# Kernel tuning notes

Measured on AMD Instinct MI355X. Metric: run time of the kernel, lower is better.

The kernel has to match this reference:

```python
import jax, jax.numpy as jnp
import numpy as np

L = 6       # n_layers
D = 1024    # d_model
H = 16      # n_heads
HD = D // H
DF = 4096   # d_ff
E = 8       # n_experts
K = 2       # top_k
V = 32000   # vocab
B = 2
S = 1024    # seq_len == max_seq_len


def setup_inputs() -> dict:
    key = jax.random.key(0)
    ks = iter(jax.random.split(key, 40))
    n = lambda shape: jax.random.normal(next(ks), shape, dtype=jnp.float32) * 0.02
    return {
        'input_ids': jax.random.randint(next(ks), (B, S), 0, V),
        'tok_emb': n((V, D)),
        'pos_emb': n((S, D)),
        'attn_in_w': n((L, 3 * D, D)),   # packed q,k,v in_proj (torch MultiheadAttention)
        'attn_in_b': jnp.zeros((L, 3 * D), jnp.float32),
        'attn_out_w': n((L, D, D)),
        'attn_out_b': jnp.zeros((L, D), jnp.float32),
        'ln1_w': jnp.ones((L, D), jnp.float32),
        'ln1_b': jnp.zeros((L, D), jnp.float32),
        'ln2_w': jnp.ones((L, D), jnp.float32),
        'ln2_b': jnp.zeros((L, D), jnp.float32),
        'ffn_w1': n((L, DF, D)),
        'ffn_b1': jnp.zeros((L, DF), jnp.float32),
        'ffn_w2': n((L, D, DF)),
        'ffn_b2': jnp.zeros((L, D), jnp.float32),
        'gate_w': n((L // 2, E, D)),     # router gate for the 3 MoE (odd) layers
        'lnf_w': jnp.ones((D,), jnp.float32),
        'lnf_b': jnp.zeros((D,), jnp.float32),
        'head_w': n((V, D)),
    }


def _ln(x, w, b):
    m = x.mean(-1, keepdims=True)
    v = x.var(-1, keepdims=True)
    return (x - m) / jnp.sqrt(v + 1e-5) * w + b


def _mha(x, in_w, in_b, out_w, out_b):
    b_, s_, _ = x.shape
    qkv = x @ in_w.T + in_b
    q, k, v = jnp.split(qkv, 3, axis=-1)
    rs = lambda t: t.reshape(b_, s_, H, HD)
    q, k, v = rs(q), rs(k), rs(v)
    scores = jnp.einsum('bqhd,bkhd->bhqk', q, k) / np.sqrt(HD).astype(np.float32)
    causal = jnp.tril(jnp.ones((s_, s_), bool))
    scores = jnp.where(causal[None, None], scores, -jnp.inf)
    a = jax.nn.softmax(scores, axis=-1)
    o = jnp.einsum('bhqk,bkhd->bqhd', a, v).reshape(b_, s_, D)
    return o @ out_w.T + out_b


def reference(input_ids, tok_emb, pos_emb, attn_in_w, attn_in_b, attn_out_w,
              attn_out_b, ln1_w, ln1_b, ln2_w, ln2_b, ffn_w1, ffn_b1, ffn_w2,
              ffn_b2, gate_w, lnf_w, lnf_b, head_w):
    s = input_ids.shape[1]
    x = tok_emb[input_ids] + pos_emb[jnp.arange(s)][None]  # [B,S,D]
    aux = jnp.float32(0.0)
    for i in range(L):
        h = _ln(x + _mha(x, attn_in_w[i], attn_in_b[i], attn_out_w[i], attn_out_b[i]),
                ln1_w[i], ln1_b[i])
        ffn = jax.nn.relu(h @ ffn_w1[i].T + ffn_b1[i]) @ ffn_w2[i].T + ffn_b2[i]
        if i % 2 == 1:  # MoE layer; source shares ONE expert module across all experts
            gi = i // 2
            probs = jax.nn.softmax(h @ gate_w[gi].T, axis=-1)     # [B,S,E]
            topv, topi = jax.lax.top_k(probs, K)
            ffn = ffn * topv.sum(-1, keepdims=True)               # combine top-k weights
            me = probs.mean((0, 1))                               # mean gate prob per expert
            ce = jax.nn.one_hot(topi[..., 0], E, dtype=probs.dtype).mean((0, 1))
            aux = aux + E * jnp.sum(me * ce)                      # load-balancing aux loss
        x = _ln(h + ffn, ln2_w[i], ln2_b[i])
    x = _ln(x, lnf_w, lnf_b)
    logits = x @ head_w.T  # [B,S,V]
    return (logits, aux)
```

## Files before the change

### kernel.cpp

```cpp
#include <hip/hip_runtime.h>
#include <hip/hip_bf16.h>

typedef __hip_bfloat16 bf16;
typedef __bf16 bf16x8 __attribute__((ext_vector_type(8)));
typedef float f32x4 __attribute__((ext_vector_type(4)));
typedef short s16x8 __attribute__((ext_vector_type(8)));
typedef unsigned short u16;

#define NL 6
#define DM 1024
#define NH 16
#define HD 64
#define DF 4096
#define NE 8
#define NV 32000
#define NB 2
#define NS 1024
#define NT (NB*NS)

__device__ __forceinline__ float ldin(const void* p, long i, int isf32) {
    return isf32 ? ((const float*)p)[i]
                 : __bfloat162float(((const bf16*)p)[i]);
}

__global__ __launch_bounds__(256)
void cvt_k(const void* __restrict__ src, bf16* __restrict__ dst, long n,
           const u16* __restrict__ probe)
{
    int isf32 = (probe[0] != (u16)0x3F80);
    long stride = (long)gridDim.x * 256 * 8;
    for (long i = ((long)blockIdx.x * 256 + threadIdx.x) * 8; i < n; i += stride) {
        if (isf32) {
            const float* s = (const float*)src + i;
            f32x4 f0 = *(const f32x4*)s;
            f32x4 f1 = *(const f32x4*)(s + 4);
            s16x8 o;
            #pragma unroll
            for (int jj = 0; jj < 4; ++jj) {
                bf16 v0 = __float2bfloat16(f0[jj]);
                bf16 v1 = __float2bfloat16(f1[jj]);
                o[jj]   = *(short*)&v0;
                o[4+jj] = *(short*)&v1;
            }
            *(s16x8*)&dst[i] = o;
        } else {
            *(s16x8*)&dst[i] = *(const s16x8*)((const u16*)src + i);
        }
    }
}

template<int TMI, int WF32, int WB16, int RELU>
__global__ __launch_bounds__(256)
void gemm128(const u16* __restrict__ A, const u16* __restrict__ B,
             const void* __restrict__ bias, long biasoff,
             const u16* __restrict__ probe,
             float* __restrict__ Cf, bf16* __restrict__ Cb,
             int M, int N, int K, int lda, int ldb, int ldc, float alpha)
{
    int isf32 = (probe[0] != (u16)0x3F80);
    int bm = blockIdx.x, bn = blockIdx.y;

    __shared__ __align__(16) u16 As[TMI*32*64];
    __shared__ __align__(16) u16 Bs[128*64];

    int t = threadIdx.x;
    int lane = t & 63, wv = t >> 6;
    int wr = wv >> 1, wc = wv & 1;
    int rsel = lane & 15, grp = lane >> 4;

    f32x4 acc[TMI][4] = {};

    const u16* Ag = A + (long)(bm * (TMI*32)) * lda;
    const u16* Bg = B + (long)(bn * 128) * ldb;
    int sub = lane >> 3;
    int csw = ((lane & 7) ^ sub) * 8;

    for (int kt = 0; kt < K; kt += 64) {
        __syncthreads();
        #pragma unroll
        for (int i = 0; i < TMI; ++i) {
            int row = wv*(TMI*8) + i*8;
            __builtin_amdgcn_global_load_lds(
                (const __attribute__((address_space(1))) void*)(Ag + (long)(row + sub)*lda + kt + csw),
                (__attribute__((address_space(3))) void*)(As + row*64),
                16, 0, 0);
        }
        #pragma unroll
        for (int i = 0; i < 4; ++i) {
            int row = wv*32 + i*8;
            __builtin_amdgcn_global_load_lds(
                (const __attribute__((address_space(1))) void*)(Bg + (long)(row + sub)*ldb + kt + csw),
                (__attribute__((address_space(3))) void*)(Bs + row*64),
                16, 0, 0);
        }
        __syncthreads();
        #pragma unroll
        for (int kk = 0; kk < 2; ++kk) {
            int js = ((kk*4 + grp) ^ (rsel & 7)) * 8;
            bf16x8 af[TMI], bf[4];
            #pragma unroll
            for (int mi = 0; mi < TMI; ++mi)
                af[mi] = *(const bf16x8*)&As[(wr*(TMI*16) + mi*16 + rsel)*64 + js];
            #pragma unroll
            for (int ni = 0; ni < 4; ++ni)
                bf[ni] = *(const bf16x8*)&Bs[(wc*64 + ni*16 + rsel)*64 + js];
            #pragma unroll
            for (int mi = 0; mi < TMI; ++mi)
                #pragma unroll
                for (int ni = 0; ni < 4; ++ni)
                    acc[mi][ni] = __builtin_amdgcn_mfma_f32_16x16x32_bf16(
                        af[mi], bf[ni], acc[mi][ni], 0, 0, 0);
        }
    }

    #pragma unroll
    for (int mi = 0; mi < TMI; ++mi)
    #pragma unroll
    for (int ni = 0; ni < 4; ++ni)
    #pragma unroll
    for (int j = 0; j < 4; ++j) {
        int row = bm*(TMI*32) + wr*(TMI*16) + mi*16 + grp*4 + j;
        int col = bn*128 + wc*64 + ni*16 + rsel;
        float v = acc[mi][ni][j] * alpha;
        if (bias) v += ldin(bias, biasoff + col, isf32);
        if (RELU) v = fmaxf(v, 0.f);
        long ci = (long)row * ldc + col;
        if (WF32) Cf[ci] = v;
        if (WB16) Cb[ci] = __float2bfloat16(v);
    }
}

__global__ __launch_bounds__(256)
void gemm64f(const u16* __restrict__ A, const void* __restrict__ B,
             const u16* __restrict__ probe, float* __restrict__ Cf,
             int M, int N, int K, int lda, int ldb, int ldc)
{
    int isf32 = (probe[0] != (u16)0x3F80);
    int bn = blockIdx.x, bm = blockIdx.y;
    __shared__ __align__(16) u16 As[64*72];
    __shared__ __align__(16) u16 Bs[64*72];
    int t = threadIdx.x;
    int lane = t & 63, wv = t >> 6;
    int wm = (wv >> 1) * 32, wn = (wv & 1) * 32;
    int rsel = lane & 15, grp = lane >> 4;
    f32x4 acc[2][2] = {};
    const u16* Ag = A + (long)(bm * 64) * lda;
    int r0 = t >> 3, c8 = (t & 7) * 8;
    for (int kt = 0; kt < K; kt += 64) {
        __syncthreads();
        #pragma unroll
        for (int p = 0; p < 2; ++p) {
            int r = r0 + 32 * p;
            *(s16x8*)&As[r*72 + c8] = *(const s16x8*)(Ag + (long)r * lda + kt + c8);
        }
        if (isf32) {
            const float* Bg = (const float*)B + (long)(bn * 64) * ldb;
            #pragma unroll
            for (int p = 0; p < 2; ++p) {
                int r = r0 + 32 * p;
                const float* src = Bg + (long)r * ldb + kt + c8;
                f32x4 f0 = *(const f32x4*)src;
                f32x4 f1 = *(const f32x4*)(src + 4);
                s16x8 o8;
                #pragma unroll
                for (int jj = 0; jj < 4; ++jj) {
                    bf16 v0 = __float2bfloat16(f0[jj]);
                    bf16 v1 = __float2bfloat16(f1[jj]);
                    o8[jj]   = *(short*)&v0;
                    o8[4+jj] = *(short*)&v1;
                }
                *(s16x8*)&Bs[r*72 + c8] = o8;
            }
        } else {
            const u16* Bg = (const u16*)B + (long)(bn * 64) * ldb;
            #pragma unroll
            for (int p = 0; p < 2; ++p) {
                int r = r0 + 32 * p;
                *(s16x8*)&Bs[r*72 + c8] = *(const s16x8*)(Bg + (long)r * ldb + kt + c8);
            }
        }
        __syncthreads();
        #pragma unroll
        for (int kk = 0; kk < 64; kk += 32) {
            bf16x8 a0 = *(const bf16x8*)&As[(wm +      rsel)*72 + kk + grp*8];
            bf16x8 a1 = *(const bf16x8*)&As[(wm + 16 + rsel)*72 + kk + grp*8];
            bf16x8 b0 = *(const bf16x8*)&Bs[(wn +      rsel)*72 + kk + grp*8];
            bf16x8 b1 = *(const bf16x8*)&Bs[(wn + 16 + rsel)*72 + kk + grp*8];
            acc[0][0] = __builtin_amdgcn_mfma_f32_16x16x32_bf16(a0, b0, acc[0][0], 0, 0, 0);
            acc[0][1] = __builtin_amdgcn_mfma_f32_16x16x32_bf16(a0, b1, acc[0][1], 0, 0, 0);
            acc[1][0] = __builtin_amdgcn_mfma_f32_16x16x32_bf16(a1, b0, acc[1][0], 0, 0, 0);
            acc[1][1] = __builtin_amdgcn_mfma_f32_16x16x32_bf16(a1, b1, acc[1][1], 0, 0, 0);
        }
    }
    #pragma unroll
    for (int mi = 0; mi < 2; ++mi)
    #pragma unroll
    for (int ni = 0; ni < 2; ++ni)
    #pragma unroll
    for (int j = 0; j < 4; ++j) {
        int row = bm*64 + wm + 16*mi + grp*4 + j;
        int col = bn*64 + wn + 16*ni + rsel;
        Cf[(long)row * ldc + col] = acc[mi][ni][j];
    }
}

__global__ __launch_bounds__(256)
void vtrans_k(const u16* __restrict__ qkv, u16* __restrict__ vt)
{
    int st = blockIdx.x;
    int z  = blockIdx.y;
    int b = z >> 4, h = z & 15;
    __shared__ u16 T[64*72];
    int t = threadIdx.x;
    int r = t >> 3, c8 = (t & 7) * 8;
    const u16* src = qkv + (long)(b*NS + st*64) * (3*DM) + 2*DM + h*HD;
    #pragma unroll
    for (int p = 0; p < 2; ++p) {
        int s = r + p*32;
        *(s16x8*)&T[s*72 + c8] = *(const s16x8*)(src + (long)s*(3*DM) + c8);
    }
    __syncthreads();
    u16* dst = vt + (long)z*HD*NS + (long)st*64;
    #pragma unroll
    for (int p = 0; p < 2; ++p) {
        int d = r + p*32;
        u16 tmp[8];
        #pragma unroll
        for (int j = 0; j < 8; ++j) tmp[j] = T[(c8+j)*72 + d];
        *(s16x8*)(dst + (long)d*NS + c8) = *(s16x8*)tmp;
    }
}

__global__ __launch_bounds__(256)
void flash_k(const u16* __restrict__ qkv, const u16* __restrict__ vt,
             bf16* __restrict__ o)
{
    int qt = blockIdx.x;
    int z  = blockIdx.y;
    int b = z >> 4, h = z & 15;

    __shared__ __align__(16) u16 Qs[64*72];
    __shared__ __align__(16) u16 Ks[2][64*64];
    __shared__ __align__(16) u16 Vs[2][64*64];
    __shared__ __align__(16) u16 Ps[4*16*72];

    int t = threadIdx.x;
    int lane = t & 63, wv = t >> 6;
    int rsel = lane & 15, grp = lane >> 4;
    int sub = lane >> 3, csw = ((lane & 7) ^ sub) * 8;

    const u16* qbase = qkv + (long)(b*NS) * (3*DM) + h*HD;
    const u16* kbase = qbase + DM;
    const u16* vbase = vt + (long)z*HD*NS;

    {
        #pragma unroll
        for (int u = 0; u < 2; ++u) {
            int id = t + u*256;
            int r = id >> 3, c = (id & 7) * 8;
            *(s16x8*)&Qs[r*72 + c] = *(const s16x8*)(qbase + (long)(qt*64 + r)*(3*DM) + c);
        }
    }

    auto stage = [&](int buf, int kt) {
        #pragma unroll
        for (int i = 0; i < 2; ++i) {
            int row = wv*16 + i*8;
            __builtin_amdgcn_global_load_lds(
                (const __attribute__((address_space(1))) void*)(kbase + (long)(kt*64 + row + sub)*(3*DM) + csw),
                (__attribute__((address_space(3))) void*)(&Ks[buf][row*64]),
                16, 0, 0);
            __builtin_amdgcn_global_load_lds(
                (const __attribute__((address_space(1))) void*)(vbase + (long)(row + sub)*NS + kt*64 + csw),
                (__attribute__((address_space(3))) void*)(&Vs[buf][row*64]),
                16, 0, 0);
        }
    };
    stage(0, 0);
    __syncthreads();

    bf16x8 qf[2];
    #pragma unroll
    for (int kk = 0; kk < 2; ++kk)
        qf[kk] = *(const bf16x8*)&Qs[(wv*16 + rsel)*72 + kk*32 + grp*8];

    float m[4], l[4];
    f32x4 acc_o[4] = {};
    #pragma unroll
    for (int j = 0; j < 4; ++j) { m[j] = -3.0e38f; l[j] = 0.f; }

    for (int kt = 0; kt <= qt; ++kt) {
        int cur = kt & 1;
        if (kt < qt) stage(cur ^ 1, kt + 1);

        f32x4 s[4] = {};
        #pragma unroll
        for (int kk = 0; kk < 2; ++kk) {
            int js = ((kk*4 + grp) ^ (rsel & 7)) * 8;
            #pragma unroll
            for (int ni = 0; ni < 4; ++ni) {
                bf16x8 bf = *(const bf16x8*)&Ks[cur][(16*ni + rsel)*64 + js];
                s[ni] = __builtin_amdgcn_mfma_f32_16x16x32_bf16(qf[kk], bf, s[ni], 0, 0, 0);
            }
        }
        float sv[4][4];
        int rloc = wv*16 + grp*4;
        #pragma unroll
        for (int ni = 0; ni < 4; ++ni)
        #pragma unroll
        for (int j = 0; j < 4; ++j) {
            float x = s[ni][j] * 0.125f;
            if (kt == qt && (16*ni + rsel) > (rloc + j)) x = -3.0e38f;
            sv[ni][j] = x;
        }
        float pm[4];
        #pragma unroll
        for (int j = 0; j < 4; ++j)
            pm[j] = fmaxf(fmaxf(sv[0][j], sv[1][j]), fmaxf(sv[2][j], sv[3][j]));
        #pragma unroll
        for (int msk = 1; msk < 16; msk <<= 1)
            #pragma unroll
            for (int j = 0; j < 4; ++j)
                pm[j] = fmaxf(pm[j], __shfl_xor(pm[j], msk));

        float mn[4], sc[4], ps[4];
        #pragma unroll
        for (int j = 0; j < 4; ++j) {
            mn[j] = fmaxf(m[j], pm[j]);
            sc[j] = __expf(m[j] - mn[j]);
            ps[j] = 0.f;
        }
        u16* pw = &Ps[wv*16*72];
        #pragma unroll
        for (int ni = 0; ni < 4; ++ni)
        #pragma unroll
        for (int j = 0; j < 4; ++j) {
            float p = __expf(sv[ni][j] - mn[j]);
            ps[j] += p;
            bf16 pb = __float2bfloat16(p);
            pw[(grp*4 + j)*72 + 16*ni + rsel] = *(u16*)&pb;
        }
        #pragma unroll
        for (int msk = 1; msk < 16; msk <<= 1)
            #pragma unroll
            for (int j = 0; j < 4; ++j)
                ps[j] += __shfl_xor(ps[j], msk);
        #pragma unroll
        for (int j = 0; j < 4; ++j) {
            l[j] = l[j]*sc[j] + ps[j];
            m[j] = mn[j];
        }
        #pragma unroll
        for (int ni = 0; ni < 4; ++ni)
        #pragma unroll
        for (int j = 0; j < 4; ++j)
            acc_o[ni][j] *= sc[j];

        __syncthreads();

        #pragma unroll
        for (int kk = 0; kk < 2; ++kk) {
            int js = ((kk*4 + grp) ^ (rsel & 7)) * 8;
            bf16x8 pa = *(const bf16x8*)&pw[rsel*72 + kk*32 + grp*8];
            #pragma unroll
            for (int ni = 0; ni < 4; ++ni) {
                bf16x8 vf = *(const bf16x8*)&Vs[cur][(16*ni + rsel)*64 + js];
                acc_o[ni] = __builtin_amdgcn_mfma_f32_16x16x32_bf16(pa, vf, acc_o[ni], 0, 0, 0);
            }
        }
        __syncthreads();
    }

    #pragma unroll
    for (int j = 0; j < 4; ++j) {
        int q = qt*64 + wv*16 + grp*4 + j;
        float inv = 1.f / l[j];
        #pragma unroll
        for (int ni = 0; ni < 4; ++ni) {
            int d = 16*ni + rsel;
            o[(long)(b*NS + q)*DM + h*HD + d] = __float2bfloat16(acc_o[ni][j] * inv);
        }
    }
}

__global__ __launch_bounds__(256)
void embed_k(const int* __restrict__ ids, const void* __restrict__ te,
             const void* __restrict__ pe, const u16* __restrict__ probe,
             float* __restrict__ xf, bf16* __restrict__ xb)
{
    int isf32 = (probe[0] != (u16)0x3F80);
    int tk = blockIdx.x;
    int s = tk & (NS-1);
    long idb = (long)ids[tk] * DM;
    #pragma unroll
    for (int u = 0; u < 4; ++u) {
        int d = threadIdx.x + u*256;
        float v = ldin(te, idb + d, isf32) + ldin(pe, (long)s*DM + d, isf32);
        xf[(long)tk*DM + d] = v;
        xb[(long)tk*DM + d] = __float2bfloat16(v);
    }
}

__global__ __launch_bounds__(256)
void ln_k(const float* __restrict__ in1, const float* __restrict__ in2,
          const float* __restrict__ rsc, const void* __restrict__ w, long woff,
          const void* __restrict__ b, long boff, const u16* __restrict__ probe,
          float* __restrict__ of, bf16* __restrict__ ob)
{
    int isf32 = (probe[0] != (u16)0x3F80);
    int row = blockIdx.x;
    int t = threadIdx.x;
    const float* p1 = in1 + (long)row * DM;
    float sc = rsc ? rsc[row] : 1.f;
    float v[4], s = 0.f;
    #pragma unroll
    for (int u = 0; u < 4; ++u) {
        int d = t + u*256;
        float x = p1[d];
        if (in2) x += sc * in2[(long)row*DM + d];
        v[u] = x; s += x;
    }
    __shared__ float r1[4], r2[4];
    int lane = t & 63, wv = t >> 6;
    #pragma unroll
    for (int msk = 32; msk; msk >>= 1) s += __shfl_xor(s, msk);
    if (lane == 0) r1[wv] = s;
    __syncthreads();
    float mean = (r1[0]+r1[1]+r1[2]+r1[3]) * (1.f/DM);
    float vs = 0.f;
    #pragma unroll
    for (int u = 0; u < 4; ++u) { float d0 = v[u] - mean; vs += d0*d0; }
    #pragma unroll
    for (int msk = 32; msk; msk >>= 1) vs += __shfl_xor(vs, msk);
    if (lane == 0) r2[wv] = vs;
    __syncthreads();
    float var = (r2[0]+r2[1]+r2[2]+r2[3]) * (1.f/DM);
    float rstd = rsqrtf(var + 1e-5f);
    #pragma unroll
    for (int u = 0; u < 4; ++u) {
        int d = t + u*256;
        float y = (v[u] - mean) * rstd * ldin(w, woff + d, isf32) + ldin(b, boff + d, isf32);
        if (of) of[(long)row*DM + d] = y;
        if (ob) ob[(long)row*DM + d] = __float2bfloat16(y);
    }
}

__global__ __launch_bounds__(256)
void router_k(const float* __restrict__ h, const void* __restrict__ gwp, long goff,
              const u16* __restrict__ probe,
              float* __restrict__ scale, float* __restrict__ mece)
{
    int isf32 = (probe[0] != (u16)0x3F80);
    int lane = threadIdx.x & 63, wv = threadIdx.x >> 6;
    int base = blockIdx.x * 64 + wv * 16;

    float me_loc[NE], ce_loc[NE];
    #pragma unroll
    for (int e = 0; e < NE; ++e) { me_loc[e] = 0.f; ce_loc[e] = 0.f; }

    for (int j = 0; j < 16; ++j) {
        int tk = base + j;
        const float* hr = h + (long)tk * DM;
        float part[NE];
        #pragma unroll
        for (int e = 0; e < NE; ++e) part[e] = 0.f;
        #pragma unroll 4
        for (int i = 0; i < 16; ++i) {
            int d = lane + 64*i;
            float hv = hr[d];
            #pragma unroll
            for (int e = 0; e < NE; ++e)
                part[e] += hv * ldin(gwp, goff + e*DM + d, isf32);
        }
        #pragma unroll
        for (int e = 0; e < NE; ++e)
            #pragma unroll
            for (int msk = 32; msk; msk >>= 1)
                part[e] += __shfl_xor(part[e], msk);
        float mx = part[0];
        #pragma unroll
        for (int e = 1; e < NE; ++e) mx = fmaxf(mx, part[e]);
        float ex[NE], sum = 0.f;
        #pragma unroll
        for (int e = 0; e < NE; ++e) { ex[e] = __expf(part[e] - mx); sum += ex[e]; }
        float inv = 1.f / sum;
        int i1 = 0; float v1 = ex[0]*inv;
        #pragma unroll
        for (int e = 1; e < NE; ++e) { float p = ex[e]*inv; if (p > v1) { v1 = p; i1 = e; } }
        float v2 = -1.f;
        #pragma unroll
        for (int e = 0; e < NE; ++e) { float p = ex[e]*inv; if (e != i1 && p > v2) v2 = p; }
        if (lane == 0) {
            scale[tk] = v1 + v2;
            #pragma unroll
            for (int e = 0; e < NE; ++e) me_loc[e] += ex[e]*inv;
            ce_loc[i1] += 1.f;
        }
    }

    __shared__ float red[4][2*NE];
    if (lane == 0) {
        #pragma unroll
        for (int e = 0; e < NE; ++e) {
            red[wv][e]      = me_loc[e];
            red[wv][NE + e] = ce_loc[e];
        }
    }
    __syncthreads();
    if (threadIdx.x < 2*NE) {
        float s = red[0][threadIdx.x] + red[1][threadIdx.x]
                + red[2][threadIdx.x] + red[3][threadIdx.x];
        atomicAdd(&mece[threadIdx.x], s);
    }
}

__global__ void auxfin_k(const float* __restrict__ me, const float* __restrict__ ce,
                         float* __restrict__ aux)
{
    float s = 0.f;
    for (int e = 0; e < NE; ++e) s += me[e] * ce[e];
    *aux += (float)NE * s * (1.f / ((float)NT * (float)NT));
}

__global__ void zerof(float* p, int n)
{
    int i = blockIdx.x * 64 + threadIdx.x;
    if (i < n) p[i] = 0.f;
}

__global__ void write_aux_f32_k(float* dst, const float* aux)
{
    *dst = *aux;
}

extern "C" void kernel_launch(void* const* d_in, const int* in_sizes, int n_in,
                              void* d_out, int out_size, void* d_ws, size_t ws_size,
                              hipStream_t stream)
{
    const int*  ids     = (const int*)d_in[0];
    const void* tok_emb = d_in[1];
    const void* pos_emb = d_in[2];
    const void* ain_w   = d_in[3];
    const void* ain_b   = d_in[4];
    const void* aout_w  = d_in[5];
    const void* aout_b  = d_in[6];
    const u16*  probe   = (const u16*)d_in[7];
    const void* ln1w    = d_in[7];
    const void* ln1b    = d_in[8];
    const void* ln2w    = d_in[9];
    const void* ln2b    = d_in[10];
    const void* fw1     = d_in[11];
    const void* fb1     = d_in[12];
    const void* fw2     = d_in[13];
    const void* fb2     = d_in[14];
    const void* gw      = d_in[15];
    const void* lnfw    = d_in[16];
    const void* lnfb    = d_in[17];
    const void* headw   = d_in[18];
    float* out = (float*)d_out;

    char* op = (char*)d_out;
    auto oalloc = [&](size_t n) { char* p = op; op += (n + 255) & ~(size_t)255; return p; };
    bf16*  f1_b   = (bf16*) oalloc((size_t)NT*DF*2);
    bf16*  qkv_b  = (bf16*) oalloc((size_t)NT*3*DM*2);
    float* tmp_f  = (float*)oalloc((size_t)NT*DM*4);
    bf16*  o_b    = (bf16*) oalloc((size_t)NT*DM*2);
    bf16*  h_b    = (bf16*) oalloc((size_t)NT*DM*2);
    float* x_f    = (float*)oalloc((size_t)NT*DM*4);
    float* h_f    = (float*)oalloc((size_t)NT*DM*4);
    u16*   vt     = (u16*)  oalloc((size_t)NB*NH*HD*NS*2);
    bf16*  wc_ain = (bf16*) oalloc((size_t)NL*3*DM*DM*2);
    bf16*  wc_aout= (bf16*) oalloc((size_t)NL*DM*DM*2);
    bf16*  wc_fw1 = (bf16*) oalloc((size_t)NL*DF*DM*2);
    bf16*  wc_fw2 = (bf16*) oalloc((size_t)NL*DM*DF*2);

    char* wp = (char*)d_ws;
    auto alloc = [&](size_t n) { char* p = wp; wp += (n + 255) & ~(size_t)255; return p; };
    bf16*  x_b    = (bf16*) alloc((size_t)NT*DM*2);
    float* scale  = (float*)alloc((size_t)NT*4);
    float* mece   = (float*)alloc(16*4);
    float* aux    = (float*)alloc(4);
    size_t ws_used = (size_t)(wp - (char*)d_ws);
    bool head_cvt = (ws_size >= ws_used + (size_t)NV*DM*2 + 256);
    bf16* wc_head = head_cvt ? (bf16*)alloc((size_t)NV*DM*2) : nullptr;

    auto cvt = [&](const void* src, bf16* dst, long n) {
        int blocks = (int)((n/8 + 255) / 256); if (blocks > 2048) blocks = 2048;
        cvt_k<<<blocks, 256, 0, stream>>>(src, dst, n, probe);
    };

    zerof<<<1, 64, 0, stream>>>(aux, 1);
    cvt(ain_w,  wc_ain,  (long)NL*3*DM*DM);
    cvt(aout_w, wc_aout, (long)NL*DM*DM);
    cvt(fw1,    wc_fw1,  (long)NL*DF*DM);
    cvt(fw2,    wc_fw2,  (long)NL*DM*DF);
    if (head_cvt) cvt(headw, wc_head, (long)NV*DM);

    embed_k<<<NT, 256, 0, stream>>>(ids, tok_emb, pos_emb, probe, x_f, x_b);

    for (int i = 0; i < NL; ++i) {
        gemm128<4,0,1,0><<<dim3(NT/128, 3*DM/128), 256, 0, stream>>>(
            (const u16*)x_b, (const u16*)(wc_ain + (size_t)i*3*DM*DM),
            ain_b, (long)i*3*DM, probe,
            nullptr, qkv_b, NT, 3*DM, DM, DM, DM, 3*DM, 1.f);
        vtrans_k<<<dim3(NS/64, NB*NH), 256, 0, stream>>>((const u16*)qkv_b, vt);
        flash_k<<<dim3(NS/64, NB*NH), 256, 0, stream>>>((const u16*)qkv_b, vt, o_b);
        gemm128<2,1,0,0><<<dim3(NT/64, DM/128), 256, 0, stream>>>(
            (const u16*)o_b, (const u16*)(wc_aout + (size_t)i*DM*DM),
            aout_b, (long)i*DM, probe,
            tmp_f, nullptr, NT, DM, DM, DM, DM, DM, 1.f);
        ln_k<<<NT, 256, 0, stream>>>(x_f, tmp_f, nullptr, ln1w, (long)i*DM, ln1b, (long)i*DM,
                                     probe, h_f, h_b);
        gemm128<4,0,1,1><<<dim3(NT/128, DF/128), 256, 0, stream>>>(
            (const u16*)h_b, (const u16*)(wc_fw1 + (size_t)i*DF*DM),
            fb1, (long)i*DF, probe,
            nullptr, f1_b, NT, DF, DM, DM, DM, DF, 1.f);
        gemm128<2,1,0,0><<<dim3(NT/64, DM/128), 256, 0, stream>>>(
            (const u16*)f1_b, (const u16*)(wc_fw2 + (size_t)i*DM*DF),
            fb2, (long)i*DM, probe,
            tmp_f, nullptr, NT, DM, DF, DF, DF, DM, 1.f);
        const float* sc = nullptr;
        if (i & 1) {
            zerof<<<1, 64, 0, stream>>>(mece, 16);
            router_k<<<NT/64, 256, 0, stream>>>(h_f, gw, (long)(i/2)*NE*DM, probe,
                                                scale, mece);
            auxfin_k<<<1, 1, 0, stream>>>(mece, mece + 8, aux);
            sc = scale;
        }
        ln_k<<<NT, 256, 0, stream>>>(h_f, tmp_f, sc, ln2w, (long)i*DM, ln2b, (long)i*DM,
                                     probe, x_f, x_b);
    }
    ln_k<<<NT, 256, 0, stream>>>(x_f, nullptr, nullptr, lnfw, 0, lnfb, 0, probe, nullptr, x_b);
    if (head_cvt) {
        gemm128<4,1,0,0><<<dim3(NT/128, NV/128), 256, 0, stream>>>(
            (const u16*)x_b, (const u16*)wc_head, nullptr, 0, probe,
            out, nullptr, NT, NV, DM, DM, DM, NV, 1.f);
    } else {
        gemm64f<<<dim3(NV/64, NT/64), 256, 0, stream>>>(
            (const u16*)x_b, headw, probe, out, NT, NV, DM, DM, DM, NV);
    }
    write_aux_f32_k<<<1, 1, 0, stream>>>(out + (size_t)NT*NV, aux);
}
```

Before: 1.939 ms.

## Process 128-key tiles in flash attention, drop double buffering and per-tile syncs

The flash attention kernel now handles keys in 128-wide chunks instead of 64, so it does half as many softmax rescale and barrier rounds per query tile. The double-buffered K/V prefetch is removed and replaced by a single synchronous load per chunk. The Q staging buffer is reused as the P scratch to save LDS, and masking is applied by global index on every chunk. The trade-off is that loads no longer overlap with compute, and diagonal chunks may do extra masked work past the causal boundary.

```diff
diff --git a/kernel.cpp b/kernel.cpp
--- a/kernel.cpp
+++ b/kernel.cpp
@@ -17,6 +17,10 @@
 #define NB 2
 #define NS 1024
 #define NT (NB*NS)
+#define NBH (NB*NH)
+
+#define AS1 __attribute__((address_space(1)))
+#define AS3 __attribute__((address_space(3)))
 
 __device__ __forceinline__ float ldin(const void* p, long i, int isf32) {
     return isf32 ? ((const float*)p)[i]
@@ -81,17 +85,15 @@
         for (int i = 0; i < TMI; ++i) {
             int row = wv*(TMI*8) + i*8;
             __builtin_amdgcn_global_load_lds(
-                (const __attribute__((address_space(1))) void*)(Ag + (long)(row + sub)*lda + kt + csw),
-                (__attribute__((address_space(3))) void*)(As + row*64),
-                16, 0, 0);
+                (const AS1 void*)(Ag + (long)(row + sub)*lda + kt + csw),
+                (AS3 void*)(As + row*64), 16, 0, 0);
         }
         #pragma unroll
         for (int i = 0; i < 4; ++i) {
             int row = wv*32 + i*8;
             __builtin_amdgcn_global_load_lds(
-                (const __attribute__((address_space(1))) void*)(Bg + (long)(row + sub)*ldb + kt + csw),
-                (__attribute__((address_space(3))) void*)(Bs + row*64),
-                16, 0, 0);
+                (const AS1 void*)(Bg + (long)(row + sub)*ldb + kt + csw),
+                (AS3 void*)(Bs + row*64), 16, 0, 0);
         }
         __syncthreads();
         #pragma unroll
@@ -238,22 +240,24 @@
     int qt = blockIdx.x;
     int z  = blockIdx.y;
     int b = z >> 4, h = z & 15;
-
-    __shared__ __align__(16) u16 Qs[64*72];
-    __shared__ __align__(16) u16 Ks[2][64*64];
-    __shared__ __align__(16) u16 Vs[2][64*64];
-    __shared__ __align__(16) u16 Ps[4*16*72];
+    int nc = (qt + 2) >> 1;
+
+    __shared__ __align__(16) u16 UPs[4*16*136];
+    __shared__ __align__(16) u16 Ks[128*64];
+    __shared__ __align__(16) u16 Vs[64*128];
 
     int t = threadIdx.x;
     int lane = t & 63, wv = t >> 6;
     int rsel = lane & 15, grp = lane >> 4;
-    int sub = lane >> 3, csw = ((lane & 7) ^ sub) * 8;
+    int sub = lane >> 3, c8s = lane & 7;
+    int sub4 = lane >> 4, c16 = lane & 15;
 
     const u16* qbase = qkv + (long)(b*NS) * (3*DM) + h*HD;
     const u16* kbase = qbase + DM;
     const u16* vbase = vt + (long)z*HD*NS;
 
     {
+        u16* Qs = UPs;
         #pragma unroll
         for (int u = 0; u < 2; ++u) {
             int id = t + u*256;
@@ -261,62 +265,68 @@
             *(s16x8*)&Qs[r*72 + c] = *(const s16x8*)(qbase + (long)(qt*64 + r)*(3*DM) + c);
         }
     }
-
-    auto stage = [&](int buf, int kt) {
-        #pragma unroll
-        for (int i = 0; i < 2; ++i) {
-            int row = wv*16 + i*8;
-            __builtin_amdgcn_global_load_lds(
-                (const __attribute__((address_space(1))) void*)(kbase + (long)(kt*64 + row + sub)*(3*DM) + csw),
-                (__attribute__((address_space(3))) void*)(&Ks[buf][row*64]),
-                16, 0, 0);
-            __builtin_amdgcn_global_load_lds(
-                (const __attribute__((address_space(1))) void*)(vbase + (long)(row + sub)*NS + kt*64 + csw),
-                (__attribute__((address_space(3))) void*)(&Vs[buf][row*64]),
-                16, 0, 0);
-        }
-    };
-    stage(0, 0);
     __syncthreads();
-
     bf16x8 qf[2];
     #pragma unroll
     for (int kk = 0; kk < 2; ++kk)
-        qf[kk] = *(const bf16x8*)&Qs[(wv*16 + rsel)*72 + kk*32 + grp*8];
+        qf[kk] = *(const bf16x8*)&UPs[(wv*16 + rsel)*72 + kk*32 + grp*8];
 
     float m[4], l[4];
     f32x4 acc_o[4] = {};
     #pragma unroll
     for (int j = 0; j < 4; ++j) { m[j] = -3.0e38f; l[j] = 0.f; }
 
-    for (int kt = 0; kt <= qt; ++kt) {
-        int cur = kt & 1;
-        if (kt < qt) stage(cur ^ 1, kt + 1);
-
-        f32x4 s[4] = {};
+    u16* pw = &UPs[wv*16*136];
+    int rloc = wv*16 + grp*4;
+    int qg = qt*64 + rloc;
+
+    for (int ci = 0; ci < nc; ++ci) {
+        __syncthreads();
+        #pragma unroll
+        for (int i = 0; i < 4; ++i) {
+            int row = wv*32 + i*8;
+            int csw = (c8s ^ sub) * 8;
+            __builtin_amdgcn_global_load_lds(
+                (const AS1 void*)(kbase + (long)(ci*128 + row + sub)*(3*DM) + csw),
+                (AS3 void*)(&Ks[row*64]), 16, 0, 0);
+        }
+        #pragma unroll
+        for (int i = 0; i < 4; ++i) {
+            int rowb = wv*16 + i*4;
+            int d = rowb + sub4;
+            int csw = (c16 ^ (d & 7)) * 8;
+            __builtin_amdgcn_global_load_lds(
+                (const AS1 void*)(vbase + (long)d*NS + ci*128 + csw),
+                (AS3 void*)(&Vs[rowb*128]), 16, 0, 0);
+        }
+        __syncthreads();
+
+        f32x4 s[8];
+        #pragma unroll
+        for (int ni = 0; ni < 8; ++ni) s[ni] = (f32x4){0.f, 0.f, 0.f, 0.f};
         #pragma unroll
         for (int kk = 0; kk < 2; ++kk) {
             int js = ((kk*4 + grp) ^ (rsel & 7)) * 8;
             #pragma unroll
-            for (int ni = 0; ni < 4; ++ni) {
-                bf16x8 bf = *(const bf16x8*)&Ks[cur][(16*ni + rsel)*64 + js];
-                s[ni] = __builtin_amdgcn_mfma_f32_16x16x32_bf16(qf[kk], bf, s[ni], 0, 0, 0);
+            for (int ni = 0; ni < 8; ++ni) {
+                bf16x8 kf = *(const bf16x8*)&Ks[(16*ni + rsel)*64 + js];
+                s[ni] = __builtin_amdgcn_mfma_f32_16x16x32_bf16(qf[kk], kf, s[ni], 0, 0, 0);
             }
         }
-        float sv[4][4];
-        int rloc = wv*16 + grp*4;
-        #pragma unroll
-        for (int ni = 0; ni < 4; ++ni)
-        #pragma unroll
-        for (int j = 0; j < 4; ++j) {
-            float x = s[ni][j] * 0.125f;
-            if (kt == qt && (16*ni + rsel) > (rloc + j)) x = -3.0e38f;
-            sv[ni][j] = x;
-        }
         float pm[4];
         #pragma unroll
-        for (int j = 0; j < 4; ++j)
-            pm[j] = fmaxf(fmaxf(sv[0][j], sv[1][j]), fmaxf(sv[2][j], sv[3][j]));
+        for (int j = 0; j < 4; ++j) pm[j] = -3.0e38f;
+        #pragma unroll
+        for (int ni = 0; ni < 8; ++ni) {
+            int kg = ci*128 + 16*ni + rsel;
+            #pragma unroll
+            for (int j = 0; j < 4; ++j) {
+                float x = s[ni][j] * 0.125f;
+                if (kg > qg + j) x = -3.0e38f;
+                s[ni][j] = x;
+                pm[j] = fmaxf(pm[j], x);
+            }
+        }
         #pragma unroll
         for (int msk = 1; msk < 16; msk <<= 1)
             #pragma unroll
@@ -330,15 +340,14 @@
             sc[j] = __expf(m[j] - mn[j]);
             ps[j] = 0.f;
         }
-        u16* pw = &Ps[wv*16*72];
-        #pragma unroll
-        for (int ni = 0; ni < 4; ++ni)
+        #pragma unroll
+        for (int ni = 0; ni < 8; ++ni)
         #pragma unroll
         for (int j = 0; j < 4; ++j) {
-            float p = __expf(sv[ni][j] - mn[j]);
+            float p = __expf(s[ni][j] - mn[j]);
             ps[j] += p;
             bf16 pb = __float2bfloat16(p);
-            pw[(grp*4 + j)*72 + 16*ni + rsel] = *(u16*)&pb;
+            pw[(grp*4 + j)*136 + 16*ni + rsel] = *(u16*)&pb;
         }
         #pragma unroll
         for (int msk = 1; msk < 16; msk <<= 1)
@@ -356,19 +365,16 @@
         for (int j = 0; j < 4; ++j)
             acc_o[ni][j] *= sc[j];
 
-        __syncthreads();
-
-        #pragma unroll
-        for (int kk = 0; kk < 2; ++kk) {
-            int js = ((kk*4 + grp) ^ (rsel & 7)) * 8;
-            bf16x8 pa = *(const bf16x8*)&pw[rsel*72 + kk*32 + grp*8];
+        #pragma unroll
+        for (int kkp = 0; kkp < 4; ++kkp) {
+            bf16x8 pa = *(const bf16x8*)&pw[rsel*136 + kkp*32 + grp*8];
+            int js = ((kkp*4 + grp) ^ (rsel & 7)) * 8;
             #pragma unroll
             for (int ni = 0; ni < 4; ++ni) {
-                bf16x8 vf = *(const bf16x8*)&Vs[cur][(16*ni + rsel)*64 + js];
+                bf16x8 vf = *(const bf16x8*)&Vs[(16*ni + rsel)*128 + js];
                 acc_o[ni] = __builtin_amdgcn_mfma_f32_16x16x32_bf16(pa, vf, acc_o[ni], 0, 0, 0);
             }
         }
-        __syncthreads();
     }
 
     #pragma unroll
@@ -568,7 +574,7 @@
     bf16*  h_b    = (bf16*) oalloc((size_t)NT*DM*2);
     float* x_f    = (float*)oalloc((size_t)NT*DM*4);
     float* h_f    = (float*)oalloc((size_t)NT*DM*4);
-    u16*   vt     = (u16*)  oalloc((size_t)NB*NH*HD*NS*2);
+    u16*   vt     = (u16*)  oalloc((size_t)NBH*HD*NS*2);
     bf16*  wc_ain = (bf16*) oalloc((size_t)NL*3*DM*DM*2);
     bf16*  wc_aout= (bf16*) oalloc((size_t)NL*DM*DM*2);
     bf16*  wc_fw1 = (bf16*) oalloc((size_t)NL*DF*DM*2);
@@ -603,8 +609,8 @@
             (const u16*)x_b, (const u16*)(wc_ain + (size_t)i*3*DM*DM),
             ain_b, (long)i*3*DM, probe,
             nullptr, qkv_b, NT, 3*DM, DM, DM, DM, 3*DM, 1.f);
-        vtrans_k<<<dim3(NS/64, NB*NH), 256, 0, stream>>>((const u16*)qkv_b, vt);
-        flash_k<<<dim3(NS/64, NB*NH), 256, 0, stream>>>((const u16*)qkv_b, vt, o_b);
+        vtrans_k<<<dim3(NS/64, NBH), 256, 0, stream>>>((const u16*)qkv_b, vt);
+        flash_k<<<dim3(NS/64, NBH), 256, 0, stream>>>((const u16*)qkv_b, vt, o_b);
         gemm128<2,1,0,0><<<dim3(NT/64, DM/128), 256, 0, stream>>>(
             (const u16*)o_b, (const u16*)(wc_aout + (size_t)i*DM*DM),
             aout_b, (long)i*DM, probe,
```

Result: no change. 1.922 ms (-0.9%).
